# Optimization experiments

Hardware: AMD Instinct MI355X
Metric: run time of the kernel (lower is better)

Reference implementation:

```python
import jax, jax.numpy as jnp
import numpy as np

RC = 5.0
N_ATYPE = 10
ACSF_NMU = 20
APSF_NMU = 10
ACSF_ETA = 100.0
APSF_ETA = 25.0
N_ATOMS = 30000
N_PAIRS = 200000
MAX_NB = 6
DENSE = 64
FEAT_DIM = ACSF_NMU * N_ATYPE + APSF_NMU * N_ATYPE + 22  # 322
ZINDEX = jnp.array([1.0, 3.0, 5.0, 6.0, 7.0, 8.0, 9.0, 11.0, 15.0, 16.0])
CHARGE_KEYS = jnp.array([0.0, 1.0, 3.0, 5.0, 6.0, 7.0, 8.0, 9.0, 11.0, 15.0, 16.0])
CHARGE_VALS = jnp.array([100000, 0, 1, 2, 3, 4, 5, 6, 7, 8, 9])


def pbc_shift(dr, box, box_inv):
    ds = dr @ box_inv
    ds = ds - jnp.floor(ds + 0.5)
    return ds @ box


def int_to_onehot(labels, num_classes):
    zidx = CHARGE_VALS[jnp.searchsorted(CHARGE_KEYS, labels)]
    return jax.nn.one_hot(zidx, num_classes, dtype=labels.dtype)


def dense_ln_relu(x, W, b, g, beta):
    h = x @ W + b
    mu = jnp.mean(h, axis=-1, keepdims=True)
    var = jnp.mean(jnp.square(h - mu), axis=-1, keepdims=True)
    return jax.nn.relu((h - mu) * jax.lax.rsqrt(var + 1e-6) * g + beta)


def forward(pos, box, valid_mask, W1, b1, g1, be1, W2, b2, g2, be2, W3, b3, g3, be3, Wo, bo,
            pairs, topo_nblist, topo_mask, mol_ID, atype_indices):
    dt = pos.dtype
    acsf_mus = jnp.linspace(0.0, 5.0, ACSF_NMU).astype(dt)
    apsf_mus = jnp.linspace(-1.0, 1.0, APSF_NMU).astype(dt)
    mScales = jnp.array([0.0, 0.0, 0.0, 0.0, 0.0, 1.0], dtype=dt)
    # regularize_pairs: padded pairs have i >= j, shift them off-diagonal
    p = pairs[:, :2]
    dp_flag = (p[:, 1] - p[:, 0] <= 0).astype(p.dtype)
    p = p - jnp.stack([dp_flag, 2 * dp_flag], axis=1)
    nbonds = pairs[:, 2]
    buffer_scales = (p[:, 0] < p[:, 1]).astype(dt) * valid_mask
    mscales = mScales[nbonds - 1] * buffer_scales  # computed as in original (unused downstream)
    box_inv = jnp.linalg.inv(box)
    ri = pos[p[:, 0]]
    rj = pos[p[:, 1]]
    rij = pbc_shift(rj - ri, box, box_inv)
    dr_norm = jnp.linalg.norm(rij + 1e-10, axis=1)
    same_mol = mol_ID[p[:, 0]] == mol_ID[p[:, 1]]
    buffer_inter = jnp.where(same_mol, 0.0, 1.0).astype(dt)
    cutoff = jnp.where(dr_norm <= RC, 0.5 * (1 + jnp.cos(jnp.pi * dr_norm / RC)), 0.0)
    buffer_nblist_inter_rc = buffer_inter * buffer_scales * cutoff
    # environment atoms of each pair endpoint (bonded topology neighbors)
    j_nb = topo_nblist[p[:, 0]]  # [P, M]
    k_nb = topo_nblist[p[:, 1]]
    j_mask = topo_mask[p[:, 0]] & (j_nb != -1) & (j_nb != p[:, 0:1]) & (j_nb != p[:, 1:2])
    k_mask = topo_mask[p[:, 1]] & (k_nb != -1) & (k_nb != p[:, 0:1]) & (k_nb != p[:, 1:2])
    rij_unit = rij / (dr_norm[:, None] + 1e-10)

    def cos_gamma(center, nb, mask, unit):
        r_env = jnp.where(mask[..., None], pos[nb], 0.0)  # [P, M, 3]
        rX = pbc_shift(r_env - center[:, None, :], box, box_inv)
        rXn = rX / jnp.linalg.norm(rX + 1e-10, axis=2, keepdims=True)
        return jnp.einsum('pmi,pi->pm', rXn, unit) * mask

    cos_gamma_i = cos_gamma(ri, j_nb, j_mask, rij_unit)
    cos_gamma_j = cos_gamma(rj, k_nb, k_mask, -rij_unit)
    type_cols = jnp.arange(N_ATYPE)

    def apsf(cg, nb, mask):
        feat = jnp.exp(-APSF_ETA * jnp.square(cg[..., None] - apsf_mus)) * mask[..., None]
        onehot = (atype_indices[nb][..., None] == type_cols).astype(dt)
        return jnp.einsum('pmk,pml->pkl', feat, onehot)  # [P, APSF_NMU, N_ATYPE]

    G_pair = (apsf(cos_gamma_i, j_nb, j_mask) + apsf(cos_gamma_j, k_nb, k_mask)) * 0.5 \
             * buffer_nblist_inter_rc[:, None, None]
    # ACSF radial atom-centered features
    r_env = pos[topo_nblist]  # [N, M, 3]
    dr = pbc_shift(r_env - pos[:, None, :], box, box_inv)
    dnorm = jnp.linalg.norm(dr + 1e-10, axis=2)
    fx = dnorm / RC
    f_cut = jnp.where(fx < 1, 0.5 * (jnp.cos(jnp.pi * fx) + 1), 0.0) * topo_mask
    G_raw = jnp.exp(-ACSF_ETA * jnp.square(dnorm[..., None] - acsf_mus)) * f_cut[..., None]
    nb_onehot = (atype_indices[topo_nblist][..., None] == type_cols).astype(dt)
    G_atom = jnp.einsum('nmk,nml->nkl', G_raw, nb_onehot)  # [N, ACSF_NMU, N_ATYPE]
    atom_feat = 0.5 * (G_atom[p[:, 0]] + G_atom[p[:, 1]])
    # element charge + one-hot block
    elem = ZINDEX[atype_indices].astype(dt)
    j_z = elem[p[:, 0]]
    k_z = elem[p[:, 1]]
    atype_onehot = jnp.concatenate([j_z[:, None], int_to_onehot(j_z, 10),
                                    k_z[:, None], int_to_onehot(k_z, 10)], axis=1)
    feats = jnp.concatenate([atom_feat.reshape(atom_feat.shape[0], -1),
                             G_pair.reshape(G_pair.shape[0], -1),
                             atype_onehot], axis=1)  # [P, 322]
    # MLP energy head
    x = dense_ln_relu(feats, W1, b1, g1, be1)
    x = dense_ln_relu(x, W2, b2, g2, be2)
    x = dense_ln_relu(x, W3, b3, g3, be3)
    out_AB = x @ Wo + bo
    return jnp.sum(out_AB * buffer_nblist_inter_rc[:, None])


def setup_inputs() -> dict:
    key = jax.random.key(0)
    ks = jax.random.split(key, 16)
    L = 30.0
    pos = jax.random.uniform(ks[0], (N_ATOMS, 3), jnp.float32, 0.0, L)
    box = jnp.eye(3, dtype=jnp.float32) * L
    i = jax.random.randint(ks[1], (N_PAIRS,), 2, N_ATOMS)
    j = jax.random.randint(ks[2], (N_PAIRS,), 2, N_ATOMS)
    p0 = jnp.minimum(i, j)
    p1 = jnp.maximum(i, j)
    pairs = jnp.stack([p0, p1, jnp.full((N_PAIRS,), 6, dtype=p0.dtype)], axis=1)
    valid_mask = (jax.random.uniform(ks[3], (N_PAIRS,)) < 0.95).astype(jnp.float32)
    nb = jax.random.randint(ks[4], (N_ATOMS, MAX_NB), 0, N_ATOMS)
    topo_nblist = jnp.where(jax.random.uniform(ks[5], (N_ATOMS, MAX_NB)) < 0.25, -1, nb)
    topo_mask = topo_nblist != -1
    mol_ID = jnp.arange(N_ATOMS, dtype=jnp.int32) // 3
    atype_indices = jax.random.randint(ks[6], (N_ATOMS,), 0, N_ATYPE)

    def dense_w(k, fin, fout):
        return jax.random.normal(k, (fin, fout), jnp.float32) / np.float32(np.sqrt(fin))

    return {
        'pos': pos, 'box': box, 'valid_mask': valid_mask,
        'W1': dense_w(ks[7], FEAT_DIM, DENSE), 'b1': jnp.zeros((DENSE,), jnp.float32),
        'g1': jnp.ones((DENSE,), jnp.float32), 'be1': jnp.zeros((DENSE,), jnp.float32),
        'W2': dense_w(ks[8], DENSE, DENSE), 'b2': jnp.zeros((DENSE,), jnp.float32),
        'g2': jnp.ones((DENSE,), jnp.float32), 'be2': jnp.zeros((DENSE,), jnp.float32),
        'W3': dense_w(ks[9], DENSE, DENSE), 'b3': jnp.zeros((DENSE,), jnp.float32),
        'g3': jnp.ones((DENSE,), jnp.float32), 'be3': jnp.zeros((DENSE,), jnp.float32),
        'Wo': dense_w(ks[10], DENSE, 1), 'bo': jnp.zeros((1,), jnp.float32),
        'pairs': pairs, 'topo_nblist': topo_nblist, 'topo_mask': topo_mask,
        'mol_ID': mol_ID, 'atype_indices': atype_indices,
    }


def reference(pos, box, valid_mask, W1, b1, g1, be1, W2, b2, g2, be2, W3, b3, g3, be3, Wo, bo,
              pairs, topo_nblist, topo_mask, mol_ID, atype_indices):
    return forward(pos, box, valid_mask, W1, b1, g1, be1, W2, b2, g2, be2, W3, b3, g3, be3, Wo, bo,
                   pairs, topo_nblist, topo_mask, mol_ID, atype_indices)
```

## Files before the change

kernel.cpp:

```cpp
#include <hip/hip_runtime.h>
#include <math.h>

#define N_PAIRS_C 200000
#define MAX_NB_C 6
#define RC_F 5.0f
#define PI_F 3.14159265358979323846f
#define NBLK 256
#define NTHR 512
#define NWAVE 8
#define SLICE 782
#define LCAP 96
#define W1S 324
#define W23S 68

__device__ __constant__ float c_ZIND[10] = {1.f, 3.f, 5.f, 6.f, 7.f, 8.f, 9.f, 11.f, 15.f, 16.f};

__device__ __forceinline__ void invert3x3(const float* b, float* inv) {
    float a00 = b[0], a01 = b[1], a02 = b[2];
    float a10 = b[3], a11 = b[4], a12 = b[5];
    float a20 = b[6], a21 = b[7], a22 = b[8];
    float det = a00 * (a11 * a22 - a12 * a21)
              - a01 * (a10 * a22 - a12 * a20)
              + a02 * (a10 * a21 - a11 * a20);
    float id = 1.0f / det;
    inv[0] =  (a11 * a22 - a12 * a21) * id;
    inv[1] = -(a01 * a22 - a02 * a21) * id;
    inv[2] =  (a01 * a12 - a02 * a11) * id;
    inv[3] = -(a10 * a22 - a12 * a20) * id;
    inv[4] =  (a00 * a22 - a02 * a20) * id;
    inv[5] = -(a00 * a12 - a02 * a10) * id;
    inv[6] =  (a10 * a21 - a11 * a20) * id;
    inv[7] = -(a00 * a21 - a01 * a20) * id;
    inv[8] =  (a00 * a11 - a01 * a10) * id;
}

__device__ __forceinline__ void pbc3(float dx, float dy, float dz,
                                     const float* box, const float* binv,
                                     float& ox, float& oy, float& oz) {
    float s0 = dx * binv[0] + dy * binv[3] + dz * binv[6];
    float s1 = dx * binv[1] + dy * binv[4] + dz * binv[7];
    float s2 = dx * binv[2] + dy * binv[5] + dz * binv[8];
    s0 -= floorf(s0 + 0.5f);
    s1 -= floorf(s1 + 0.5f);
    s2 -= floorf(s2 + 0.5f);
    ox = s0 * box[0] + s1 * box[3] + s2 * box[6];
    oy = s0 * box[1] + s1 * box[4] + s2 * box[7];
    oz = s0 * box[2] + s1 * box[5] + s2 * box[8];
}

__device__ __forceinline__ float wsum64(float v) {
    #pragma unroll
    for (int off = 32; off > 0; off >>= 1) v += __shfl_xor(v, off, 64);
    return v;
}

__device__ __forceinline__ float ln_relu(float h, float g, float be) {
    float mu = wsum64(h) * 0.015625f;
    float d  = h - mu;
    float var = wsum64(d * d) * 0.015625f;
    float r = d * (1.0f / sqrtf(var + 1e-6f)) * g + be;
    return fmaxf(r, 0.0f);
}

__device__ __forceinline__ float rlf(float v, int lane) {
    return __int_as_float(__builtin_amdgcn_readlane(__float_as_int(v), lane));
}
__device__ __forceinline__ int rli(int v, int lane) {
    return __builtin_amdgcn_readlane(v, lane);
}

__global__ __launch_bounds__(NTHR) void fused_kernel(
    const float* __restrict__ pos,
    const float* __restrict__ box,
    const float* __restrict__ valid_mask,
    const float* __restrict__ W1, const float* __restrict__ b1,
    const float* __restrict__ g1, const float* __restrict__ be1,
    const float* __restrict__ W2, const float* __restrict__ b2,
    const float* __restrict__ g2, const float* __restrict__ be2,
    const float* __restrict__ W3, const float* __restrict__ b3,
    const float* __restrict__ g3, const float* __restrict__ be3,
    const float* __restrict__ Wo, const float* __restrict__ bo,
    const int* __restrict__ pairs,
    const int* __restrict__ nblist,
    const int* __restrict__ atype,
    const int* __restrict__ mol_ID,
    float* __restrict__ out) {

    __shared__ __align__(16) float W1t[64][W1S];
    __shared__ __align__(16) float W2t[64][W23S];
    __shared__ __align__(16) float W3t[64][W23S];
    __shared__ int   l_p0[LCAP], l_p1[LCAP];
    __shared__ float l_fac[LCAP];
    __shared__ int   l_cnt;
    __shared__ float wacc[NWAVE];

    const int tid = threadIdx.x;
    const int w = tid >> 6;
    const int j = tid & 63;
    const int a8 = (j >> 3) & 7;

    if (tid == 0) l_cnt = 0;

    float bx[9], bi[9];
    #pragma unroll
    for (int i = 0; i < 9; ++i) bx[i] = box[i];
    invert3x3(bx, bi);

    for (int q = w; q < 81; q += NWAVE) {
        int qs = (q < 80) ? ((q & ~7) | ((q ^ a8) & 7)) : 80;
        int f0 = 4 * q;
        float4 v;
        v.x = W1[(f0 + 0) * 64 + j];
        v.y = W1[(f0 + 1) * 64 + j];
        v.z = (f0 + 2 < 322) ? W1[(f0 + 2) * 64 + j] : 0.0f;
        v.w = (f0 + 3 < 322) ? W1[(f0 + 3) * 64 + j] : 0.0f;
        *(float4*)&W1t[j][4 * qs] = v;
    }
    for (int q = w; q < 16; q += NWAVE) {
        int qs = (q & 8) | ((q ^ a8) & 7);
        int f0 = 4 * q;
        float4 v2, v3;
        v2.x = W2[(f0 + 0) * 64 + j]; v3.x = W3[(f0 + 0) * 64 + j];
        v2.y = W2[(f0 + 1) * 64 + j]; v3.y = W3[(f0 + 1) * 64 + j];
        v2.z = W2[(f0 + 2) * 64 + j]; v3.z = W3[(f0 + 2) * 64 + j];
        v2.w = W2[(f0 + 3) * 64 + j]; v3.w = W3[(f0 + 3) * 64 + j];
        *(float4*)&W2t[j][4 * qs] = v2;
        *(float4*)&W3t[j][4 * qs] = v3;
    }
    __syncthreads();

    {
        int tb = blockIdx.x * SLICE;
        int lim = tb + SLICE;
        if (lim > N_PAIRS_C) lim = N_PAIRS_C;
        for (int t = tb + tid; t < lim; t += NTHR) {
            int i0 = pairs[3 * t], i1 = pairs[3 * t + 1];
            int dp = (i1 - i0 <= 0) ? 1 : 0;
            int p0 = i0 - dp, p1 = i1 - 2 * dp;
            if (p0 >= p1) continue;
            float vm = valid_mask[t];
            if (vm == 0.0f) continue;
            if (mol_ID[p0] == mol_ID[p1]) continue;
            float dx, dy, dz;
            pbc3(pos[3 * p1] - pos[3 * p0],
                 pos[3 * p1 + 1] - pos[3 * p0 + 1],
                 pos[3 * p1 + 2] - pos[3 * p0 + 2], bx, bi, dx, dy, dz);
            float ax = dx + 1e-10f, ay = dy + 1e-10f, az = dz + 1e-10f;
            float dn = sqrtf(ax * ax + ay * ay + az * az);
            if (dn > RC_F) continue;
            float fac = vm * 0.5f * (1.0f + __cosf(PI_F * dn / RC_F));
            int slot = atomicAdd(&l_cnt, 1);
            if (slot < LCAP) { l_p0[slot] = p0; l_p1[slot] = p1; l_fac[slot] = fac; }
        }
    }
    __syncthreads();

    int cnt = l_cnt;
    if (cnt > LCAP) cnt = LCAP;

    float mu_[5];
    int ty_[5], selr_[5];
    #pragma unroll
    for (int r = 0; r < 5; ++r) {
        int F = j + 64 * r;
        if (F < 200)      { mu_[r] = 5.0f * (float)(F / 10) / 19.0f; ty_[r] = F % 10; selr_[r] = 1; }
        else if (F < 300) { int G = F - 200; mu_[r] = -1.0f + 2.0f * (float)(G / 10) / 9.0f; ty_[r] = G % 10; selr_[r] = 0; }
        else              { mu_[r] = 0.0f; ty_[r] = 255; selr_[r] = 0; }
    }

    const float b1j = b1[j], g1j = g1[j], be1j = be1[j];
    const float b2j = b2[j], g2j = g2[j], be2j = be2[j];
    const float b3j = b3[j], g3j = g3[j], be3j = be3[j];
    const float woj = Wo[j], bo0 = bo[0];

    const float* w1row = &W1t[j][0];
    const float* w2row = &W2t[j][0];
    const float* w3row = &W3t[j][0];

    float acc = 0.0f;

    #pragma unroll 1
    for (int base = 0; base < cnt; base += 2 * NWAVE) {
        int iA = base + 2 * w;
        if (iA >= cnt) break;
        int iB = iA + 1;
        bool okB = iB < cnt;
        int p0A = l_p0[iA], p1A = l_p1[iA]; float facA = l_fac[iA];
        int p0B = okB ? l_p0[iB] : p0A, p1B = okB ? l_p1[iB] : p1A;
        float facB = okB ? l_fac[iB] : 0.0f;

        int tiA = atype[p0A], tjA = atype[p1A];
        int tiB = atype[p0B], tjB = atype[p1B];

        float sdn = 1.0f, sfce = 0.0f, scg = 0.0f, sapw = 0.0f;
        int sty = 0;
        {
            bool isA = (j < 12);
            bool isB = (j >= 16 && j < 28);
            if (isA || isB) {
                int s  = isA ? j : (j - 16);
                int p0 = isA ? p0A : p0B;
                int p1 = isA ? p1A : p1B;
                float fac = isA ? facA : facB;
                float rix = pos[3 * p0], riy = pos[3 * p0 + 1], riz = pos[3 * p0 + 2];
                float rjx = pos[3 * p1], rjy = pos[3 * p1 + 1], rjz = pos[3 * p1 + 2];
                float dxr, dyr, dzr;
                pbc3(rjx - rix, rjy - riy, rjz - riz, bx, bi, dxr, dyr, dzr);
                float axr = dxr + 1e-10f, ayr = dyr + 1e-10f, azr = dzr + 1e-10f;
                float dn0 = sqrtf(axr * axr + ayr * ayr + azr * azr);
                float idn = 1.0f / (dn0 + 1e-10f);
                float ux = dxr * idn, uy = dyr * idn, uz = dzr * idn;
                int side = (s >= 6) ? 1 : 0;
                int m = side ? (s - 6) : s;
                int a = side ? p1 : p0;
                int nb = nblist[a * MAX_NB_C + m];
                if (nb != -1) {
                    float cx = side ? rjx : rix;
                    float cy = side ? rjy : riy;
                    float cz = side ? rjz : riz;
                    float ex, ey, ez;
                    pbc3(pos[3 * nb] - cx, pos[3 * nb + 1] - cy, pos[3 * nb + 2] - cz,
                         bx, bi, ex, ey, ez);
                    float nx = ex + 1e-10f, ny = ey + 1e-10f, nz = ez + 1e-10f;
                    float dn = sqrtf(nx * nx + ny * ny + nz * nz);
                    float fr2 = dn * (1.0f / RC_F);
                    float fc = (fr2 < 1.0f) ? 0.5f * (__cosf(PI_F * fr2) + 1.0f) : 0.0f;
                    sdn = dn;
                    sfce = 0.5f * fc;
                    sty = atype[nb];
                    int pv = (nb != p0 && nb != p1) ? 1 : 0;
                    float sgn = side ? -1.0f : 1.0f;
                    scg = sgn * (ex * ux + ey * uy + ez * uz) / dn;
                    sapw = pv ? 0.5f * fac : 0.0f;
                }
            }
        }

        float frA[6] = {0.f, 0.f, 0.f, 0.f, 0.f, 0.f};
        float frB[6] = {0.f, 0.f, 0.f, 0.f, 0.f, 0.f};
        #pragma unroll 1
        for (int s = 0; s < 12; ++s) {
            float dnA = rlf(sdn, s),      feA = rlf(sfce, s);
            float cgA = rlf(scg, s),      awA = rlf(sapw, s);
            float dnB = rlf(sdn, 16 + s), feB = rlf(sfce, 16 + s);
            float cgB = rlf(scg, 16 + s), awB = rlf(sapw, 16 + s);
            int tA = rli(sty, s), tB = rli(sty, 16 + s);
            #pragma unroll
            for (int r = 0; r < 5; ++r) {
                float e = selr_[r] ? -100.0f : -25.0f;
                {
                    float x = selr_[r] ? dnA : cgA, wg = selr_[r] ? feA : awA, td = x - mu_[r];
                    frA[r] += ((tA == ty_[r]) ? wg : 0.0f) * __expf(e * td * td);
                }
                {
                    float x = selr_[r] ? dnB : cgB, wg = selr_[r] ? feB : awB, td = x - mu_[r];
                    frB[r] += ((tB == ty_[r]) ? wg : 0.0f) * __expf(e * td * td);
                }
            }
        }
        if (j >= 44) {
            int oh = j - 44;
            float vA, vB;
            if (oh == 0)       { vA = c_ZIND[tiA]; vB = c_ZIND[tiB]; }
            else if (oh <= 10) { vA = (tiA == oh - 1) ? 1.f : 0.f; vB = (tiB == oh - 1) ? 1.f : 0.f; }
            else if (oh == 11) { vA = c_ZIND[tjA]; vB = c_ZIND[tjB]; }
            else               { vA = (tjA == oh - 12) ? 1.f : 0.f; vB = (tjB == oh - 12) ? 1.f : 0.f; }
            frA[4] = vA; frB[4] = vB;
        }
        if (j == 0) { frA[5] = (tjA == 8) ? 1.f : 0.f; frB[5] = (tjB == 8) ? 1.f : 0.f; }
        if (j == 1) { frA[5] = (tjA == 9) ? 1.f : 0.f; frB[5] = (tjB == 9) ? 1.f : 0.f; }

        float hA = b1j, hB = b1j;
        #pragma unroll
        for (int r = 0; r < 5; ++r) {
            #pragma unroll 2
            for (int gg = 0; gg < 16; ++gg) {
                int sgg = (gg & 8) | ((gg ^ a8) & 7);
                float4 wv = ((const float4*)(w1row + 4 * sgg))[16 * r];
                int l0 = 4 * gg;
                float sA0 = rlf(frA[r], l0 + 0), sA1 = rlf(frA[r], l0 + 1);
                float sA2 = rlf(frA[r], l0 + 2), sA3 = rlf(frA[r], l0 + 3);
                float sB0 = rlf(frB[r], l0 + 0), sB1 = rlf(frB[r], l0 + 1);
                float sB2 = rlf(frB[r], l0 + 2), sB3 = rlf(frB[r], l0 + 3);
                hA = fmaf(sA0, wv.x, hA); hB = fmaf(sB0, wv.x, hB);
                hA = fmaf(sA1, wv.y, hA); hB = fmaf(sB1, wv.y, hB);
                hA = fmaf(sA2, wv.z, hA); hB = fmaf(sB2, wv.z, hB);
                hA = fmaf(sA3, wv.w, hA); hB = fmaf(sB3, wv.w, hB);
            }
        }
        {
            float w320 = w1row[320], w321 = w1row[321];
            float tA0 = rlf(frA[5], 0), tA1 = rlf(frA[5], 1);
            float tB0 = rlf(frB[5], 0), tB1 = rlf(frB[5], 1);
            hA = fmaf(tA0, w320, hA); hA = fmaf(tA1, w321, hA);
            hB = fmaf(tB0, w320, hB); hB = fmaf(tB1, w321, hB);
        }
        float x1A = ln_relu(hA, g1j, be1j);
        float x1B = ln_relu(hB, g1j, be1j);

        float h2A = b2j, h2B = b2j;
        #pragma unroll 2
        for (int gg = 0; gg < 16; ++gg) {
            int sgg = (gg & 8) | ((gg ^ a8) & 7);
            float4 wv = ((const float4*)(w2row + 4 * sgg))[0];
            int l0 = 4 * gg;
            float sA0 = rlf(x1A, l0 + 0), sA1 = rlf(x1A, l0 + 1);
            float sA2 = rlf(x1A, l0 + 2), sA3 = rlf(x1A, l0 + 3);
            float sB0 = rlf(x1B, l0 + 0), sB1 = rlf(x1B, l0 + 1);
            float sB2 = rlf(x1B, l0 + 2), sB3 = rlf(x1B, l0 + 3);
            h2A = fmaf(sA0, wv.x, h2A); h2B = fmaf(sB0, wv.x, h2B);
            h2A = fmaf(sA1, wv.y, h2A); h2B = fmaf(sB1, wv.y, h2B);
            h2A = fmaf(sA2, wv.z, h2A); h2B = fmaf(sB2, wv.z, h2B);
            h2A = fmaf(sA3, wv.w, h2A); h2B = fmaf(sB3, wv.w, h2B);
        }
        float x2A = ln_relu(h2A, g2j, be2j);
        float x2B = ln_relu(h2B, g2j, be2j);

        float h3A = b3j, h3B = b3j;
        #pragma unroll 2
        for (int gg = 0; gg < 16; ++gg) {
            int sgg = (gg & 8) | ((gg ^ a8) & 7);
            float4 wv = ((const float4*)(w3row + 4 * sgg))[0];
            int l0 = 4 * gg;
            float sA0 = rlf(x2A, l0 + 0), sA1 = rlf(x2A, l0 + 1);
            float sA2 = rlf(x2A, l0 + 2), sA3 = rlf(x2A, l0 + 3);
            float sB0 = rlf(x2B, l0 + 0), sB1 = rlf(x2B, l0 + 1);
            float sB2 = rlf(x2B, l0 + 2), sB3 = rlf(x2B, l0 + 3);
            h3A = fmaf(sA0, wv.x, h3A); h3B = fmaf(sB0, wv.x, h3B);
            h3A = fmaf(sA1, wv.y, h3A); h3B = fmaf(sB1, wv.y, h3B);
            h3A = fmaf(sA2, wv.z, h3A); h3B = fmaf(sB2, wv.z, h3B);
            h3A = fmaf(sA3, wv.w, h3A); h3B = fmaf(sB3, wv.w, h3B);
        }
        float x3A = ln_relu(h3A, g3j, be3j);
        float x3B = ln_relu(h3B, g3j, be3j);

        float rA = wsum64(x3A * woj);
        float rB = wsum64(x3B * woj);
        if (j == 0)
            acc += (rA + bo0) * facA + (rB + bo0) * facB;
    }

    if (j == 0) wacc[w] = acc;
    __syncthreads();
    if (tid == 0) {
        float tot = 0.0f;
        #pragma unroll
        for (int i = 0; i < NWAVE; ++i) tot += wacc[i];
        atomicAdd(out, tot);
    }
}

extern "C" void kernel_launch(void* const* d_in, const int* in_sizes, int n_in,
                              void* d_out, int out_size, void* d_ws, size_t ws_size,
                              hipStream_t stream) {
    const float* pos        = (const float*)d_in[0];
    const float* box        = (const float*)d_in[1];
    const float* valid_mask = (const float*)d_in[2];
    const float* W1  = (const float*)d_in[3];
    const float* b1  = (const float*)d_in[4];
    const float* g1  = (const float*)d_in[5];
    const float* be1 = (const float*)d_in[6];
    const float* W2  = (const float*)d_in[7];
    const float* b2  = (const float*)d_in[8];
    const float* g2  = (const float*)d_in[9];
    const float* be2 = (const float*)d_in[10];
    const float* W3  = (const float*)d_in[11];
    const float* b3  = (const float*)d_in[12];
    const float* g3  = (const float*)d_in[13];
    const float* be3 = (const float*)d_in[14];
    const float* Wo  = (const float*)d_in[15];
    const float* bo  = (const float*)d_in[16];
    const int* pairs = (const int*)d_in[17];
    const int* nbl   = (const int*)d_in[18];
    const int* mol   = (const int*)d_in[20];
    const int* aty   = (const int*)d_in[21];

    float* out = (float*)d_out;

    (void)hipMemsetAsync(out, 0, sizeof(float), stream);
    fused_kernel<<<NBLK, NTHR, 0, stream>>>(
        pos, box, valid_mask,
        W1, b1, g1, be1, W2, b2, g2, be2, W3, b3, g3, be3, Wo, bo,
        pairs, nbl, aty, mol, out);
}
```

Before: 47.36 us.

## Read W1 from global memory and process one pair per wave with more blocks

```diff
diff --git a/kernel.cpp b/kernel.cpp
--- a/kernel.cpp
+++ b/kernel.cpp
@@ -5,12 +5,11 @@
 #define MAX_NB_C 6
 #define RC_F 5.0f
 #define PI_F 3.14159265358979323846f
-#define NBLK 256
+#define NBLK 512
 #define NTHR 512
 #define NWAVE 8
-#define SLICE 782
-#define LCAP 96
-#define W1S 324
+#define SLICE 391
+#define LCAP 64
 #define W23S 68
 
 __device__ __constant__ float c_ZIND[10] = {1.f, 3.f, 5.f, 6.f, 7.f, 8.f, 9.f, 11.f, 15.f, 16.f};
@@ -86,7 +85,6 @@
     const int* __restrict__ mol_ID,
     float* __restrict__ out) {
 
-    __shared__ __align__(16) float W1t[64][W1S];
     __shared__ __align__(16) float W2t[64][W23S];
     __shared__ __align__(16) float W3t[64][W23S];
     __shared__ int   l_p0[LCAP], l_p1[LCAP];
@@ -97,7 +95,6 @@
     const int tid = threadIdx.x;
     const int w = tid >> 6;
     const int j = tid & 63;
-    const int a8 = (j >> 3) & 7;
 
     if (tid == 0) l_cnt = 0;
 
@@ -106,26 +103,15 @@
     for (int i = 0; i < 9; ++i) bx[i] = box[i];
     invert3x3(bx, bi);
 
-    for (int q = w; q < 81; q += NWAVE) {
-        int qs = (q < 80) ? ((q & ~7) | ((q ^ a8) & 7)) : 80;
-        int f0 = 4 * q;
-        float4 v;
-        v.x = W1[(f0 + 0) * 64 + j];
-        v.y = W1[(f0 + 1) * 64 + j];
-        v.z = (f0 + 2 < 322) ? W1[(f0 + 2) * 64 + j] : 0.0f;
-        v.w = (f0 + 3 < 322) ? W1[(f0 + 3) * 64 + j] : 0.0f;
-        *(float4*)&W1t[j][4 * qs] = v;
-    }
     for (int q = w; q < 16; q += NWAVE) {
-        int qs = (q & 8) | ((q ^ a8) & 7);
         int f0 = 4 * q;
         float4 v2, v3;
         v2.x = W2[(f0 + 0) * 64 + j]; v3.x = W3[(f0 + 0) * 64 + j];
         v2.y = W2[(f0 + 1) * 64 + j]; v3.y = W3[(f0 + 1) * 64 + j];
         v2.z = W2[(f0 + 2) * 64 + j]; v3.z = W3[(f0 + 2) * 64 + j];
         v2.w = W2[(f0 + 3) * 64 + j]; v3.w = W3[(f0 + 3) * 64 + j];
-        *(float4*)&W2t[j][4 * qs] = v2;
-        *(float4*)&W3t[j][4 * qs] = v3;
+        *(float4*)&W2t[j][f0] = v2;
+        *(float4*)&W3t[j][f0] = v3;
     }
     __syncthreads();
 
@@ -158,14 +144,14 @@
     int cnt = l_cnt;
     if (cnt > LCAP) cnt = LCAP;
 
-    float mu_[5];
+    float mu_[5], eta_[5];
     int ty_[5], selr_[5];
     #pragma unroll
     for (int r = 0; r < 5; ++r) {
         int F = j + 64 * r;
-        if (F < 200)      { mu_[r] = 5.0f * (float)(F / 10) / 19.0f; ty_[r] = F % 10; selr_[r] = 1; }
-        else if (F < 300) { int G = F - 200; mu_[r] = -1.0f + 2.0f * (float)(G / 10) / 9.0f; ty_[r] = G % 10; selr_[r] = 0; }
-        else              { mu_[r] = 0.0f; ty_[r] = 255; selr_[r] = 0; }
+        if (F < 200)      { mu_[r] = 5.0f * (float)(F / 10) / 19.0f; eta_[r] = -100.0f; ty_[r] = F % 10; selr_[r] = 1; }
+        else if (F < 300) { int G = F - 200; mu_[r] = -1.0f + 2.0f * (float)(G / 10) / 9.0f; eta_[r] = -25.0f; ty_[r] = G % 10; selr_[r] = 0; }
+        else              { mu_[r] = 0.0f; eta_[r] = 0.0f; ty_[r] = 255; selr_[r] = 0; }
     }
 
     const float b1j = b1[j], g1j = g1[j], be1j = be1[j];
@@ -173,171 +159,134 @@
     const float b3j = b3[j], g3j = g3[j], be3j = be3[j];
     const float woj = Wo[j], bo0 = bo[0];
 
-    const float* w1row = &W1t[j][0];
+    const float* W1j = W1 + j;
     const float* w2row = &W2t[j][0];
     const float* w3row = &W3t[j][0];
 
     float acc = 0.0f;
 
     #pragma unroll 1
-    for (int base = 0; base < cnt; base += 2 * NWAVE) {
-        int iA = base + 2 * w;
-        if (iA >= cnt) break;
-        int iB = iA + 1;
-        bool okB = iB < cnt;
-        int p0A = l_p0[iA], p1A = l_p1[iA]; float facA = l_fac[iA];
-        int p0B = okB ? l_p0[iB] : p0A, p1B = okB ? l_p1[iB] : p1A;
-        float facB = okB ? l_fac[iB] : 0.0f;
-
-        int tiA = atype[p0A], tjA = atype[p1A];
-        int tiB = atype[p0B], tjB = atype[p1B];
+    for (int base = 0; base < cnt; base += NWAVE) {
+        int ip = base + w;
+        if (ip >= cnt) continue;
+        int p0 = l_p0[ip], p1 = l_p1[ip];
+        float fac = l_fac[ip];
+        int ti = atype[p0], tj = atype[p1];
 
         float sdn = 1.0f, sfce = 0.0f, scg = 0.0f, sapw = 0.0f;
         int sty = 0;
-        {
-            bool isA = (j < 12);
-            bool isB = (j >= 16 && j < 28);
-            if (isA || isB) {
-                int s  = isA ? j : (j - 16);
-                int p0 = isA ? p0A : p0B;
-                int p1 = isA ? p1A : p1B;
-                float fac = isA ? facA : facB;
-                float rix = pos[3 * p0], riy = pos[3 * p0 + 1], riz = pos[3 * p0 + 2];
-                float rjx = pos[3 * p1], rjy = pos[3 * p1 + 1], rjz = pos[3 * p1 + 2];
-                float dxr, dyr, dzr;
-                pbc3(rjx - rix, rjy - riy, rjz - riz, bx, bi, dxr, dyr, dzr);
-                float axr = dxr + 1e-10f, ayr = dyr + 1e-10f, azr = dzr + 1e-10f;
-                float dn0 = sqrtf(axr * axr + ayr * ayr + azr * azr);
-                float idn = 1.0f / (dn0 + 1e-10f);
-                float ux = dxr * idn, uy = dyr * idn, uz = dzr * idn;
-                int side = (s >= 6) ? 1 : 0;
-                int m = side ? (s - 6) : s;
-                int a = side ? p1 : p0;
-                int nb = nblist[a * MAX_NB_C + m];
-                if (nb != -1) {
-                    float cx = side ? rjx : rix;
-                    float cy = side ? rjy : riy;
-                    float cz = side ? rjz : riz;
-                    float ex, ey, ez;
-                    pbc3(pos[3 * nb] - cx, pos[3 * nb + 1] - cy, pos[3 * nb + 2] - cz,
-                         bx, bi, ex, ey, ez);
-                    float nx = ex + 1e-10f, ny = ey + 1e-10f, nz = ez + 1e-10f;
-                    float dn = sqrtf(nx * nx + ny * ny + nz * nz);
-                    float fr2 = dn * (1.0f / RC_F);
-                    float fc = (fr2 < 1.0f) ? 0.5f * (__cosf(PI_F * fr2) + 1.0f) : 0.0f;
-                    sdn = dn;
-                    sfce = 0.5f * fc;
-                    sty = atype[nb];
-                    int pv = (nb != p0 && nb != p1) ? 1 : 0;
-                    float sgn = side ? -1.0f : 1.0f;
-                    scg = sgn * (ex * ux + ey * uy + ez * uz) / dn;
-                    sapw = pv ? 0.5f * fac : 0.0f;
-                }
+        if (j < 12) {
+            float rix = pos[3 * p0], riy = pos[3 * p0 + 1], riz = pos[3 * p0 + 2];
+            float rjx = pos[3 * p1], rjy = pos[3 * p1 + 1], rjz = pos[3 * p1 + 2];
+            float dxr, dyr, dzr;
+            pbc3(rjx - rix, rjy - riy, rjz - riz, bx, bi, dxr, dyr, dzr);
+            float axr = dxr + 1e-10f, ayr = dyr + 1e-10f, azr = dzr + 1e-10f;
+            float dn0 = sqrtf(axr * axr + ayr * ayr + azr * azr);
+            float idn = 1.0f / (dn0 + 1e-10f);
+            float ux = dxr * idn, uy = dyr * idn, uz = dzr * idn;
+            int side = (j >= 6) ? 1 : 0;
+            int m = side ? (j - 6) : j;
+            int a = side ? p1 : p0;
+            int nb = nblist[a * MAX_NB_C + m];
+            if (nb != -1) {
+                float cx = side ? rjx : rix;
+                float cy = side ? rjy : riy;
+                float cz = side ? rjz : riz;
+                float ex, ey, ez;
+                pbc3(pos[3 * nb] - cx, pos[3 * nb + 1] - cy, pos[3 * nb + 2] - cz,
+                     bx, bi, ex, ey, ez);
+                float nx = ex + 1e-10f, ny = ey + 1e-10f, nz = ez + 1e-10f;
+                float dn = sqrtf(nx * nx + ny * ny + nz * nz);
+                float fr2 = dn * (1.0f / RC_F);
+                float fc = (fr2 < 1.0f) ? 0.5f * (__cosf(PI_F * fr2) + 1.0f) : 0.0f;
+                sdn = dn;
+                sfce = 0.5f * fc;
+                sty = atype[nb];
+                int pv = (nb != p0 && nb != p1) ? 1 : 0;
+                float sgn = side ? -1.0f : 1.0f;
+                scg = sgn * (ex * ux + ey * uy + ez * uz) / dn;
+                sapw = pv ? 0.5f * fac : 0.0f;
             }
         }
 
-        float frA[6] = {0.f, 0.f, 0.f, 0.f, 0.f, 0.f};
-        float frB[6] = {0.f, 0.f, 0.f, 0.f, 0.f, 0.f};
+        float fr[6] = {0.f, 0.f, 0.f, 0.f, 0.f, 0.f};
         #pragma unroll 1
         for (int s = 0; s < 12; ++s) {
-            float dnA = rlf(sdn, s),      feA = rlf(sfce, s);
-            float cgA = rlf(scg, s),      awA = rlf(sapw, s);
-            float dnB = rlf(sdn, 16 + s), feB = rlf(sfce, 16 + s);
-            float cgB = rlf(scg, 16 + s), awB = rlf(sapw, 16 + s);
-            int tA = rli(sty, s), tB = rli(sty, 16 + s);
+            float dn = rlf(sdn, s), fe = rlf(sfce, s);
+            float cg = rlf(scg, s), aw = rlf(sapw, s);
+            int ty = rli(sty, s);
             #pragma unroll
             for (int r = 0; r < 5; ++r) {
-                float e = selr_[r] ? -100.0f : -25.0f;
-                {
-                    float x = selr_[r] ? dnA : cgA, wg = selr_[r] ? feA : awA, td = x - mu_[r];
-                    frA[r] += ((tA == ty_[r]) ? wg : 0.0f) * __expf(e * td * td);
-                }
-                {
-                    float x = selr_[r] ? dnB : cgB, wg = selr_[r] ? feB : awB, td = x - mu_[r];
-                    frB[r] += ((tB == ty_[r]) ? wg : 0.0f) * __expf(e * td * td);
-                }
+                float x  = selr_[r] ? dn : cg;
+                float wg = selr_[r] ? fe : aw;
+                float td = x - mu_[r];
+                fr[r] += ((ty == ty_[r]) ? wg : 0.0f) * __expf(eta_[r] * td * td);
             }
         }
         if (j >= 44) {
             int oh = j - 44;
-            float vA, vB;
-            if (oh == 0)       { vA = c_ZIND[tiA]; vB = c_ZIND[tiB]; }
-            else if (oh <= 10) { vA = (tiA == oh - 1) ? 1.f : 0.f; vB = (tiB == oh - 1) ? 1.f : 0.f; }
-            else if (oh == 11) { vA = c_ZIND[tjA]; vB = c_ZIND[tjB]; }
-            else               { vA = (tjA == oh - 12) ? 1.f : 0.f; vB = (tjB == oh - 12) ? 1.f : 0.f; }
-            frA[4] = vA; frB[4] = vB;
-        }
-        if (j == 0) { frA[5] = (tjA == 8) ? 1.f : 0.f; frB[5] = (tjB == 8) ? 1.f : 0.f; }
-        if (j == 1) { frA[5] = (tjA == 9) ? 1.f : 0.f; frB[5] = (tjB == 9) ? 1.f : 0.f; }
-
-        float hA = b1j, hB = b1j;
+            float v;
+            if (oh == 0)       v = c_ZIND[ti];
+            else if (oh <= 10) v = (ti == oh - 1) ? 1.f : 0.f;
+            else if (oh == 11) v = c_ZIND[tj];
+            else               v = (tj == oh - 12) ? 1.f : 0.f;
+            fr[4] = v;
+        }
+        if (j == 0) fr[5] = (tj == 8) ? 1.f : 0.f;
+        if (j == 1) fr[5] = (tj == 9) ? 1.f : 0.f;
+
+        float h = b1j;
         #pragma unroll
         for (int r = 0; r < 5; ++r) {
             #pragma unroll 2
-            for (int gg = 0; gg < 16; ++gg) {
-                int sgg = (gg & 8) | ((gg ^ a8) & 7);
-                float4 wv = ((const float4*)(w1row + 4 * sgg))[16 * r];
-                int l0 = 4 * gg;
-                float sA0 = rlf(frA[r], l0 + 0), sA1 = rlf(frA[r], l0 + 1);
-                float sA2 = rlf(frA[r], l0 + 2), sA3 = rlf(frA[r], l0 + 3);
-                float sB0 = rlf(frB[r], l0 + 0), sB1 = rlf(frB[r], l0 + 1);
-                float sB2 = rlf(frB[r], l0 + 2), sB3 = rlf(frB[r], l0 + 3);
-                hA = fmaf(sA0, wv.x, hA); hB = fmaf(sB0, wv.x, hB);
-                hA = fmaf(sA1, wv.y, hA); hB = fmaf(sB1, wv.y, hB);
-                hA = fmaf(sA2, wv.z, hA); hB = fmaf(sB2, wv.z, hB);
-                hA = fmaf(sA3, wv.w, hA); hB = fmaf(sB3, wv.w, hB);
+            for (int k8 = 0; k8 < 8; ++k8) {
+                const float* wp = W1j + (64 * r + 8 * k8) * 64;
+                float w0 = wp[0],   w1 = wp[64],  w2 = wp[128], w3 = wp[192];
+                float w4 = wp[256], w5 = wp[320], w6 = wp[384], w7 = wp[448];
+                int l0 = 8 * k8;
+                float s0 = rlf(fr[r], l0 + 0), s1 = rlf(fr[r], l0 + 1);
+                float s2 = rlf(fr[r], l0 + 2), s3 = rlf(fr[r], l0 + 3);
+                float s4 = rlf(fr[r], l0 + 4), s5 = rlf(fr[r], l0 + 5);
+                float s6 = rlf(fr[r], l0 + 6), s7 = rlf(fr[r], l0 + 7);
+                h = fmaf(s0, w0, h); h = fmaf(s1, w1, h);
+                h = fmaf(s2, w2, h); h = fmaf(s3, w3, h);
+                h = fmaf(s4, w4, h); h = fmaf(s5, w5, h);
+                h = fmaf(s6, w6, h); h = fmaf(s7, w7, h);
             }
         }
         {
-            float w320 = w1row[320], w321 = w1row[321];
-            float tA0 = rlf(frA[5], 0), tA1 = rlf(frA[5], 1);
-            float tB0 = rlf(frB[5], 0), tB1 = rlf(frB[5], 1);
-            hA = fmaf(tA0, w320, hA); hA = fmaf(tA1, w321, hA);
-            hB = fmaf(tB0, w320, hB); hB = fmaf(tB1, w321, hB);
-        }
-        float x1A = ln_relu(hA, g1j, be1j);
-        float x1B = ln_relu(hB, g1j, be1j);
-
-        float h2A = b2j, h2B = b2j;
+            float w320 = W1j[320 * 64], w321 = W1j[321 * 64];
+            float t0 = rlf(fr[5], 0), t1 = rlf(fr[5], 1);
+            h = fmaf(t0, w320, h); h = fmaf(t1, w321, h);
+        }
+        float x1 = ln_relu(h, g1j, be1j);
+
+        float h2 = b2j;
         #pragma unroll 2
         for (int gg = 0; gg < 16; ++gg) {
-            int sgg = (gg & 8) | ((gg ^ a8) & 7);
-            float4 wv = ((const float4*)(w2row + 4 * sgg))[0];
+            float4 wv = *(const float4*)(w2row + 4 * gg);
             int l0 = 4 * gg;
-            float sA0 = rlf(x1A, l0 + 0), sA1 = rlf(x1A, l0 + 1);
-            float sA2 = rlf(x1A, l0 + 2), sA3 = rlf(x1A, l0 + 3);
-            float sB0 = rlf(x1B, l0 + 0), sB1 = rlf(x1B, l0 + 1);
-            float sB2 = rlf(x1B, l0 + 2), sB3 = rlf(x1B, l0 + 3);
-            h2A = fmaf(sA0, wv.x, h2A); h2B = fmaf(sB0, wv.x, h2B);
-            h2A = fmaf(sA1, wv.y, h2A); h2B = fmaf(sB1, wv.y, h2B);
-            h2A = fmaf(sA2, wv.z, h2A); h2B = fmaf(sB2, wv.z, h2B);
-            h2A = fmaf(sA3, wv.w, h2A); h2B = fmaf(sB3, wv.w, h2B);
-        }
-        float x2A = ln_relu(h2A, g2j, be2j);
-        float x2B = ln_relu(h2B, g2j, be2j);
-
-        float h3A = b3j, h3B = b3j;
+            float s0 = rlf(x1, l0 + 0), s1 = rlf(x1, l0 + 1);
+            float s2 = rlf(x1, l0 + 2), s3 = rlf(x1, l0 + 3);
+            h2 = fmaf(s0, wv.x, h2); h2 = fmaf(s1, wv.y, h2);
+            h2 = fmaf(s2, wv.z, h2); h2 = fmaf(s3, wv.w, h2);
+        }
+        float x2 = ln_relu(h2, g2j, be2j);
+
+        float h3 = b3j;
         #pragma unroll 2
         for (int gg = 0; gg < 16; ++gg) {
-            int sgg = (gg & 8) | ((gg ^ a8) & 7);
-            float4 wv = ((const float4*)(w3row + 4 * sgg))[0];
+            float4 wv = *(const float4*)(w3row + 4 * gg);
             int l0 = 4 * gg;
-            float sA0 = rlf(x2A, l0 + 0), sA1 = rlf(x2A, l0 + 1);
-            float sA2 = rlf(x2A, l0 + 2), sA3 = rlf(x2A, l0 + 3);
-            float sB0 = rlf(x2B, l0 + 0), sB1 = rlf(x2B, l0 + 1);
-            float sB2 = rlf(x2B, l0 + 2), sB3 = rlf(x2B, l0 + 3);
-            h3A = fmaf(sA0, wv.x, h3A); h3B = fmaf(sB0, wv.x, h3B);
-            h3A = fmaf(sA1, wv.y, h3A); h3B = fmaf(sB1, wv.y, h3B);
-            h3A = fmaf(sA2, wv.z, h3A); h3B = fmaf(sB2, wv.z, h3B);
-            h3A = fmaf(sA3, wv.w, h3A); h3B = fmaf(sB3, wv.w, h3B);
-        }
-        float x3A = ln_relu(h3A, g3j, be3j);
-        float x3B = ln_relu(h3B, g3j, be3j);
-
-        float rA = wsum64(x3A * woj);
-        float rB = wsum64(x3B * woj);
-        if (j == 0)
-            acc += (rA + bo0) * facA + (rB + bo0) * facB;
+            float s0 = rlf(x2, l0 + 0), s1 = rlf(x2, l0 + 1);
+            float s2 = rlf(x2, l0 + 2), s3 = rlf(x2, l0 + 3);
+            h3 = fmaf(s0, wv.x, h3); h3 = fmaf(s1, wv.y, h3);
+            h3 = fmaf(s2, wv.z, h3); h3 = fmaf(s3, wv.w, h3);
+        }
+        float x3 = ln_relu(h3, g3j, be3j);
+
+        float rsum = wsum64(x3 * woj);
+        if (j == 0) acc += (rsum + bo0) * fac;
     }
 
     if (j == 0) wacc[w] = acc;
```

Measured after the change: 53.41 us. 12.8% more time.
